# Optimization experiments

Hardware: AMD Instinct MI355X
Metric: run time of the kernel (lower is better)

## Reference

```python
import jax, jax.numpy as jnp
import numpy as np

N = 100000   # nodes
E = 600000   # edges
D = 128      # hidden_dim
R = 8        # edge_vocab_size (num_relations)
B = 64       # graphs in batch
V = 5000     # node_vocab_size
L = 3        # num_layers


def setup_inputs() -> dict:
    key = jax.random.key(0)
    ks = jax.random.split(key, 16)
    s = 1.0 / np.sqrt(D)
    node_type = jax.random.randint(ks[0], (N,), 0, V, dtype=jnp.int32)
    edge_index = jax.random.randint(ks[1], (2, E), 0, N, dtype=jnp.int32)
    edge_type = jax.random.randint(ks[2], (E,), 0, R, dtype=jnp.int32)
    batch = jnp.sort(jax.random.randint(ks[3], (N,), 0, B, dtype=jnp.int32))
    node_emb = jax.random.normal(ks[4], (V, D), dtype=jnp.float32)
    rel_w = jax.random.normal(ks[5], (L, R, D, D), dtype=jnp.float32) * s
    root_w = jax.random.normal(ks[6], (L, D, D), dtype=jnp.float32) * s
    bias = jnp.zeros((L, D), dtype=jnp.float32)
    risk_w1 = jax.random.normal(ks[7], (D, D), dtype=jnp.float32) * s
    risk_b1 = jnp.zeros((D,), dtype=jnp.float32)
    risk_w2 = jax.random.normal(ks[8], (D, 1), dtype=jnp.float32) * s
    risk_b2 = jnp.zeros((1,), dtype=jnp.float32)
    safe_w1 = jax.random.normal(ks[9], (D, D), dtype=jnp.float32) * s
    safe_b1 = jnp.zeros((D,), dtype=jnp.float32)
    safe_w2 = jax.random.normal(ks[10], (D, 1), dtype=jnp.float32) * s
    safe_b2 = jnp.zeros((1,), dtype=jnp.float32)
    return dict(node_type=node_type, edge_index=edge_index, edge_type=edge_type,
                batch=batch, node_emb=node_emb, rel_w=rel_w, root_w=root_w,
                bias=bias, risk_w1=risk_w1, risk_b1=risk_b1, risk_w2=risk_w2,
                risk_b2=risk_b2, safe_w1=safe_w1, safe_b1=safe_b1,
                safe_w2=safe_w2, safe_b2=safe_b2)


def _rgcn_layer(x, edge_index, edge_type, Wrel, Wroot, b):
    # PyG RGCNConv: per-relation mean aggregation of source features,
    # then relation-specific linear + root transform + bias.
    src, dst = edge_index[0], edge_index[1]
    seg = dst * R + edge_type                      # combined (node, relation) id
    msgs = x[src]                                  # [E, D] gather
    sums = jax.ops.segment_sum(msgs, seg, num_segments=N * R)      # [N*R, D]
    cnt = jax.ops.segment_sum(jnp.ones((E,), x.dtype), seg, num_segments=N * R)
    mean = sums / jnp.maximum(cnt, 1.0)[:, None]
    mean = mean.reshape(N, R, D)
    out = jnp.einsum('nrd,rde->ne', mean, Wrel) + x @ Wroot + b
    return out


def _mlp_head(g, w1, b1, w2, b2):
    h = jax.nn.relu(g @ w1 + b1)
    return (h @ w2 + b2).squeeze(-1)               # dropout is identity in eval


def reference(node_type, edge_index, edge_type, batch, node_emb, rel_w, root_w,
              bias, risk_w1, risk_b1, risk_w2, risk_b2, safe_w1, safe_b1,
              safe_w2, safe_b2):
    x = node_emb[node_type]                        # [N, D]
    for l in range(L):                             # fixed small layer loop
        x = jax.nn.relu(_rgcn_layer(x, edge_index, edge_type,
                                    rel_w[l], root_w[l], bias[l]))
    # global_mean_pool over graph ids
    g_sum = jax.ops.segment_sum(x, batch, num_segments=B)          # [B, D]
    g_cnt = jax.ops.segment_sum(jnp.ones((N,), x.dtype), batch, num_segments=B)
    g = g_sum / jnp.maximum(g_cnt, 1.0)[:, None]
    risk_pred = _mlp_head(g, risk_w1, risk_b1, risk_w2, risk_b2)   # [B]
    safe_logit = _mlp_head(g, safe_w1, safe_b1, safe_w2, safe_b2)  # [B]
    return risk_pred, safe_logit
```

## Files before the change

### kernel.cpp

```cpp
#include <hip/hip_runtime.h>
#include <hip/hip_bf16.h>

#define N_NODES 100000
#define N_EDGES 600000
#define DIM     128
#define N_REL   8
#define N_GRAPH 64
#define N_LAYER 3
#define NR      (N_NODES * N_REL)
#define OVF_CAP 16384

typedef __attribute__((ext_vector_type(4))) float float4v;
typedef __attribute__((ext_vector_type(2))) float float2v;
typedef unsigned long long ull;

__device__ __forceinline__ int gswz8(int row, int g) {
    return row * 16 + (g ^ (row & 15));
}

#define W8_TOTAL (N_LAYER * 9 * 8192)
#define PB_HIST  2344
#define PB_GATH  12500
#define PB_WPRE  864
#define PB_BCNT  1
#define PB_TOTAL (PB_HIST + PB_GATH + PB_WPRE + PB_BCNT)

__global__ __launch_bounds__(256) void k_prep(
    const int* __restrict__ ei, const int* __restrict__ et,
    int* __restrict__ cnt, int* __restrict__ srcs8,
    int* __restrict__ ovf, int* __restrict__ ovf_n,
    const int* __restrict__ nt, const float* __restrict__ emb, unsigned int* __restrict__ x8,
    const float* __restrict__ relw, const float* __restrict__ rootw,
    unsigned short* __restrict__ W8,
    const int* __restrict__ batch, int* __restrict__ gcnt)
{
    const int b = blockIdx.x, t = threadIdx.x;
    if (b < PB_HIST) {
        int e = b * 256 + t;
        if (e < N_EDGES) {
            int src = ei[e];
            int seg = ei[N_EDGES + e] * N_REL + et[e];
            int p = atomicAdd(&cnt[seg], 1);
            if (p < 8) {
                srcs8[seg * 8 + p] = src;
            } else {
                int q = atomicAdd(ovf_n, 1);
                if (q < OVF_CAP) { ovf[2 * q] = seg; ovf[2 * q + 1] = src; }
            }
        }
    } else if (b < PB_HIST + PB_GATH) {
        int gid = (b - PB_HIST) * 256 + t;
        int n = gid >> 5, up = gid & 31;
        const float* row = emb + (size_t)nt[n] * DIM;
        int p0 = up * 4;
        float f0 = row[((p0 + 0) & 7) * 16 + ((p0 + 0) >> 3)];
        float f1 = row[((p0 + 1) & 7) * 16 + ((p0 + 1) >> 3)];
        float f2 = row[((p0 + 2) & 7) * 16 + ((p0 + 2) >> 3)];
        float f3 = row[((p0 + 3) & 7) * 16 + ((p0 + 3) >> 3)];
        int u = __builtin_amdgcn_cvt_pk_fp8_f32(f0, f1, 0, false);
        u = __builtin_amdgcn_cvt_pk_fp8_f32(f2, f3, u, true);
        x8[gid] = (unsigned int)u;
    } else if (b < PB_HIST + PB_GATH + PB_WPRE) {
        int gid = (b - PB_HIST - PB_GATH) * 256 + t;
        int l = gid / (9 * 8192);
        int rem = gid - l * 9 * 8192;
        int r = rem >> 13;
        int idx = rem & 8191;
        int n = idx >> 6, p2 = idx & 63;
        int pos0 = 2 * p2, pos1 = 2 * p2 + 1;
        int k0 = (pos0 & 7) * 16 + (pos0 >> 3);
        int k1 = (pos1 & 7) * 16 + (pos1 >> 3);
        float w0, w1;
        if (r < 8) {
            const float* base = relw + ((size_t)(l * 8 + r) * 128) * 128 + n;
            w0 = base[(size_t)k0 * 128];
            w1 = base[(size_t)k1 * 128];
        } else {
            const float* base = rootw + (size_t)l * 128 * 128 + n;
            w0 = base[(size_t)k0 * 128];
            w1 = base[(size_t)k1 * 128];
        }
        int pk = __builtin_amdgcn_cvt_pk_fp8_f32(w0, w1, 0, false);
        W8[gid] = (unsigned short)(pk & 0xffff);
    } else {
        int g = t;
        if (g < N_GRAPH) {
            int lo = 0, hi = N_NODES;
            while (lo < hi) { int mid = (lo + hi) >> 1; if (batch[mid] < g) lo = mid + 1; else hi = mid; }
            int start = lo;
            lo = 0; hi = N_NODES;
            while (lo < hi) { int mid = (lo + hi) >> 1; if (batch[mid] < g + 1) lo = mid + 1; else hi = mid; }
            gcnt[g] = lo - start;
        }
    }
}

#define BM2 128
__global__ __launch_bounds__(256, 2) void k_gemm(
    const unsigned int* __restrict__ x8in,
    unsigned int* __restrict__ x8out,
    const unsigned short* __restrict__ W8,
    const float* __restrict__ bias,
    const int* __restrict__ cnt,
    const int* __restrict__ srcs8,
    const int* __restrict__ ovf,
    const int* __restrict__ ovf_n,
    const int* __restrict__ batch,
    float* __restrict__ gsum,
    int isLast)
{
    __shared__ __align__(16) ull Bls[4096];
    __shared__ __align__(16) ull Als[2048];
    const int t = threadIdx.x;
    const int wv = t >> 6, lane = t & 63;
    const int quad = lane >> 4, l15 = lane & 15;
    const int oct = lane >> 3, h = lane & 7;
    const int m0 = blockIdx.x * BM2;
    const int gn = m0 + wv * 32 + (lane >> 1);
    const int nodeC = (gn < N_NODES) ? gn : 0;
    const int f = lane & 1;

    float4v acc[2][8];
#pragma unroll
    for (int nt = 0; nt < 8; ++nt) {
        float bc = bias[nt * 16 + l15];
        acc[0][nt] = (float4v){bc, bc, bc, bc};
        acc[1][nt] = (float4v){bc, bc, bc, bc};
    }

    const ull* Xr = (const ull*)x8in;
    const uint4* x4p = (const uint4*)x8in;
    ull* AlsW = Als + wv * 512;
    uint4* Als4 = (uint4*)AlsW;

    ull bR[8], aR[8];
    uint4 u0[4], u1[4];
    int cc[4], s2v[4], s3v[4];

#define ACCUM(U) do {                                                  \
        A0 += __builtin_amdgcn_cvt_pk_f32_fp8((int)(U).x, false);      \
        A1 += __builtin_amdgcn_cvt_pk_f32_fp8((int)(U).x, true);       \
        A2 += __builtin_amdgcn_cvt_pk_f32_fp8((int)(U).y, false);      \
        A3 += __builtin_amdgcn_cvt_pk_f32_fp8((int)(U).y, true);       \
        A4 += __builtin_amdgcn_cvt_pk_f32_fp8((int)(U).z, false);      \
        A5 += __builtin_amdgcn_cvt_pk_f32_fp8((int)(U).z, true);       \
        A6 += __builtin_amdgcn_cvt_pk_f32_fp8((int)(U).w, false);      \
        A7 += __builtin_amdgcn_cvt_pk_f32_fp8((int)(U).w, true);       \
    } while (0)

    auto ld_meta = [&](int rr, int& cl, int& s0, int& s2) {
        int seg = nodeC * 8 + rr;
        cl = cnt[seg];
        s0 = srcs8[seg * 8 + f];
        s2 = srcs8[seg * 8 + 2 + f];
    };
    auto gat_issue = [&](int cl, int sl0, int sl2) {
#pragma unroll
        for (int nn = 0; nn < 4; ++nn) {
            int lw = nn * 8 + oct;
            cc[nn] = __shfl(cl, lw * 2);
            int s0 = __shfl(sl0, lw * 2);
            int s1 = __shfl(sl0, lw * 2 + 1);
            s2v[nn] = __shfl(sl2, lw * 2);
            s3v[nn] = __shfl(sl2, lw * 2 + 1);
            if (cc[nn] > 0) u0[nn] = x4p[(size_t)s0 * 8 + h];
            if (cc[nn] > 1) u1[nn] = x4p[(size_t)s1 * 8 + h];
        }
    };
    auto agg_consume = [&](int rr) {
        uint4 u2[4], u3[4];
#pragma unroll
        for (int nn = 0; nn < 4; ++nn) {
            if (cc[nn] > 2) u2[nn] = x4p[(size_t)s2v[nn] * 8 + h];
            if (cc[nn] > 3) u3[nn] = x4p[(size_t)s3v[nn] * 8 + h];
        }
#pragma unroll
        for (int nn = 0; nn < 4; ++nn) {
            int lw = nn * 8 + oct;
            float2v A0 = {0.f, 0.f}, A1 = {0.f, 0.f}, A2 = {0.f, 0.f}, A3 = {0.f, 0.f};
            float2v A4 = {0.f, 0.f}, A5 = {0.f, 0.f}, A6 = {0.f, 0.f}, A7 = {0.f, 0.f};
            if (cc[nn] > 0) ACCUM(u0[nn]);
            if (cc[nn] > 1) ACCUM(u1[nn]);
            if (cc[nn] > 2) ACCUM(u2[nn]);
            if (cc[nn] > 3) ACCUM(u3[nn]);
            if (cc[nn] > 4) {
                int seg = (m0 + wv * 32 + lw) * 8 + rr;
                int mc = cc[nn] < 8 ? cc[nn] : 8;
#pragma unroll 1
                for (int k = 4; k < mc; ++k) {
                    uint4 uu = x4p[(size_t)srcs8[seg * 8 + k] * 8 + h];
                    ACCUM(uu);
                }
                if (cc[nn] > 8) {
                    int ovn = ovf_n[0];
                    if (ovn > OVF_CAP) ovn = OVF_CAP;
#pragma unroll 1
                    for (int j = 0; j < ovn; ++j) {
                        if (ovf[2 * j] == seg) {
                            uint4 uu = x4p[(size_t)ovf[2 * j + 1] * 8 + h];
                            ACCUM(uu);
                        }
                    }
                }
            }
            float inv = (cc[nn] > 0) ? 1.0f / (float)cc[nn] : 0.f;
            float2v iv = {inv, inv};
            A0 *= iv; A1 *= iv; A2 *= iv; A3 *= iv;
            A4 *= iv; A5 *= iv; A6 *= iv; A7 *= iv;
            int w0 = __builtin_amdgcn_cvt_pk_fp8_f32(A0.x, A0.y, 0, false);
            w0 = __builtin_amdgcn_cvt_pk_fp8_f32(A1.x, A1.y, w0, true);
            int w1 = __builtin_amdgcn_cvt_pk_fp8_f32(A2.x, A2.y, 0, false);
            w1 = __builtin_amdgcn_cvt_pk_fp8_f32(A3.x, A3.y, w1, true);
            int w2 = __builtin_amdgcn_cvt_pk_fp8_f32(A4.x, A4.y, 0, false);
            w2 = __builtin_amdgcn_cvt_pk_fp8_f32(A5.x, A5.y, w2, true);
            int w3 = __builtin_amdgcn_cvt_pk_fp8_f32(A6.x, A6.y, 0, false);
            w3 = __builtin_amdgcn_cvt_pk_fp8_f32(A7.x, A7.y, w3, true);
            uint4 w; w.x = (unsigned int)w0; w.y = (unsigned int)w1;
            w.z = (unsigned int)w2; w.w = (unsigned int)w3;
            Als4[(lw >> 4) * 128 + h * 16 + ((lw & 15) ^ h)] = w;
        }
    };

    {
        const ull* Wc = (const ull*)W8;
#pragma unroll
        for (int i = 0; i < 8; ++i) bR[i] = Wc[t + 256 * i];
    }
    int clA, sl0A, sl2A, clN, sl0N, sl2N;
    ld_meta(0, clA, sl0A, sl2A);
    gat_issue(clA, sl0A, sl2A);
    ld_meta(1, clA, sl0A, sl2A);
#pragma unroll
    for (int i = 0; i < 8; ++i) {
        int idx = t + 256 * i;
        Bls[gswz8(idx >> 4, idx & 15)] = bR[i];
    }
    __syncthreads();

#pragma unroll
    for (int c = 0; c < 9; ++c) {
        const int cur = (c & 1) * 2048;
        if (c <= 7) agg_consume(c);
        if (c <= 5) ld_meta(c + 2, clN, sl0N, sl2N);
        if (c <= 6) gat_issue(clA, sl0A, sl2A);
        if (c < 8) {
            const ull* Wc = (const ull*)(W8 + (size_t)(c + 1) * 8192);
#pragma unroll
            for (int i = 0; i < 8; ++i) bR[i] = Wc[t + 256 * i];
        }
        if (c == 7) {
#pragma unroll
            for (int i = 0; i < 8; ++i) {
                int rt = i >> 2, kk = i & 3;
                aR[i] = Xr[(size_t)(m0 + wv * 32 + rt * 16 + l15) * 16 + kk * 4 + quad];
            }
        }
#pragma unroll
        for (int kk = 0; kk < 4; ++kk) {
            long long a0, a1;
            if (c == 8) {
                a0 = (long long)aR[kk];
                a1 = (long long)aR[4 + kk];
            } else {
                int j4 = kk * 4 + quad;
                int h2 = j4 >> 1, hf = j4 & 1;
                int slot = ((h2 * 16 + (l15 ^ h2)) << 1) | hf;
                a0 = (long long)AlsW[slot];
                a1 = (long long)AlsW[256 + slot];
            }
            int g = kk * 4 + quad;
#pragma unroll
            for (int nt = 0; nt < 8; ++nt) {
                long long b8 = (long long)Bls[cur + (nt * 16 + l15) * 16 + (g ^ l15)];
                acc[0][nt] = __builtin_amdgcn_mfma_f32_16x16x32_fp8_fp8(a0, b8, acc[0][nt], 0, 0, 0);
                acc[1][nt] = __builtin_amdgcn_mfma_f32_16x16x32_fp8_fp8(a1, b8, acc[1][nt], 0, 0, 0);
            }
        }
        if (c < 8) {
            const int nxt = ((c + 1) & 1) * 2048;
#pragma unroll
            for (int i = 0; i < 8; ++i) {
                int idx = t + 256 * i;
                Bls[nxt + gswz8(idx >> 4, idx & 15)] = bR[i];
            }
            __syncthreads();
        }
        clA = clN; sl0A = sl0N; sl2A = sl2N;
    }
#undef ACCUM

    if (!isLast) {
        ull* outs = (ull*)x8out;
#pragma unroll
        for (int rt = 0; rt < 2; ++rt) {
#pragma unroll
            for (int i = 0; i < 4; ++i) {
                int row = m0 + wv * 32 + rt * 16 + quad * 4 + i;
                float v0 = acc[rt][0][i], v1 = acc[rt][1][i];
                float v2 = acc[rt][2][i], v3 = acc[rt][3][i];
                float v4 = acc[rt][4][i], v5 = acc[rt][5][i];
                float v6 = acc[rt][6][i], v7 = acc[rt][7][i];
                v0 = v0 > 0.f ? v0 : 0.f;  v1 = v1 > 0.f ? v1 : 0.f;
                v2 = v2 > 0.f ? v2 : 0.f;  v3 = v3 > 0.f ? v3 : 0.f;
                v4 = v4 > 0.f ? v4 : 0.f;  v5 = v5 > 0.f ? v5 : 0.f;
                v6 = v6 > 0.f ? v6 : 0.f;  v7 = v7 > 0.f ? v7 : 0.f;
                int lo = __builtin_amdgcn_cvt_pk_fp8_f32(v0, v1, 0, false);
                lo = __builtin_amdgcn_cvt_pk_fp8_f32(v2, v3, lo, true);
                int hi = __builtin_amdgcn_cvt_pk_fp8_f32(v4, v5, 0, false);
                hi = __builtin_amdgcn_cvt_pk_fp8_f32(v6, v7, hi, true);
                if (row < N_NODES) {
                    ull w = ((ull)(unsigned int)hi << 32) | (unsigned int)lo;
                    outs[(size_t)row * 16 + l15] = w;
                }
            }
        }
    } else {
        float s[8];
#pragma unroll
        for (int nt = 0; nt < 8; ++nt) s[nt] = 0.f;
        int curg = -1;
#pragma unroll
        for (int rt = 0; rt < 2; ++rt) {
#pragma unroll
            for (int i = 0; i < 4; ++i) {
                int row = m0 + wv * 32 + rt * 16 + quad * 4 + i;
                if (row < N_NODES) {
                    int gb = batch[row];
                    if (gb != curg) {
                        if (curg >= 0) {
#pragma unroll
                            for (int nt = 0; nt < 8; ++nt)
                                atomicAdd(&gsum[curg * 128 + nt * 16 + l15], s[nt]);
#pragma unroll
                            for (int nt = 0; nt < 8; ++nt) s[nt] = 0.f;
                        }
                        curg = gb;
                    }
#pragma unroll
                    for (int nt = 0; nt < 8; ++nt) {
                        float v = acc[rt][nt][i];
                        s[nt] += v > 0.f ? v : 0.f;
                    }
                }
            }
        }
        if (curg >= 0) {
#pragma unroll
            for (int nt = 0; nt < 8; ++nt)
                atomicAdd(&gsum[curg * 128 + nt * 16 + l15], s[nt]);
        }
    }
}

__global__ __launch_bounds__(128) void k_heads(
    const float* __restrict__ gsum, const int* __restrict__ gcnt,
    const float* __restrict__ rw1, const float* __restrict__ rb1,
    const float* __restrict__ rw2, const float* __restrict__ rb2,
    const float* __restrict__ sw1, const float* __restrict__ sb1,
    const float* __restrict__ sw2, const float* __restrict__ sb2,
    float* __restrict__ out) {
    __shared__ float g[128];
    __shared__ float parts[2];
    int b = blockIdx.x, t = threadIdx.x;
    int c = gcnt[b];
    float invc = 1.0f / (float)(c > 0 ? c : 1);
    g[t] = gsum[b * 128 + t] * invc;
    __syncthreads();
    float acc = rb1[t];
    for (int d = 0; d < 128; ++d) acc += g[d] * rw1[d * 128 + t];
    float h = acc > 0.f ? acc : 0.f;
    float p = h * rw2[t];
    for (int o = 32; o > 0; o >>= 1) p += __shfl_down(p, o);
    if ((t & 63) == 0) parts[t >> 6] = p;
    __syncthreads();
    if (t == 0) out[b] = parts[0] + parts[1] + rb2[0];
    __syncthreads();
    acc = sb1[t];
    for (int d = 0; d < 128; ++d) acc += g[d] * sw1[d * 128 + t];
    h = acc > 0.f ? acc : 0.f;
    p = h * sw2[t];
    for (int o = 32; o > 0; o >>= 1) p += __shfl_down(p, o);
    if ((t & 63) == 0) parts[t >> 6] = p;
    __syncthreads();
    if (t == 0) out[64 + b] = parts[0] + parts[1] + sb2[0];
}

extern "C" void kernel_launch(void* const* d_in, const int* in_sizes, int n_in,
                              void* d_out, int out_size, void* d_ws, size_t ws_size,
                              hipStream_t stream) {
    const int*   node_type  = (const int*)d_in[0];
    const int*   edge_index = (const int*)d_in[1];
    const int*   edge_type  = (const int*)d_in[2];
    const int*   batch      = (const int*)d_in[3];
    const float* node_emb   = (const float*)d_in[4];
    const float* rel_w      = (const float*)d_in[5];
    const float* root_w     = (const float*)d_in[6];
    const float* bias       = (const float*)d_in[7];
    const float* rw1        = (const float*)d_in[8];
    const float* rb1        = (const float*)d_in[9];
    const float* rw2        = (const float*)d_in[10];
    const float* rb2        = (const float*)d_in[11];
    const float* sw1        = (const float*)d_in[12];
    const float* sb1        = (const float*)d_in[13];
    const float* sw2        = (const float*)d_in[14];
    const float* sb2        = (const float*)d_in[15];
    float* out = (float*)d_out;

    char* ws = (char*)d_ws;
    size_t off = 0;
    auto alloc = [&](size_t bytes) -> void* {
        void* p = ws + off;
        off += (bytes + 255) & ~(size_t)255;
        return p;
    };
    unsigned int*   x8a    = (unsigned int*)alloc((size_t)N_NODES * 32 * 4);
    unsigned int*   x8b    = (unsigned int*)alloc((size_t)N_NODES * 32 * 4);
    int*            cnt    = (int*)alloc((size_t)NR * 4);
    int*            srcs8  = (int*)alloc((size_t)NR * 8 * 4);
    int*            ovf    = (int*)alloc((size_t)OVF_CAP * 2 * 4);
    unsigned short* W8     = (unsigned short*)alloc((size_t)W8_TOTAL * 2);
    float*          gsum   = (float*)alloc((64 * 128 + 64 + 64) * 4);
    int*            gcnt   = (int*)(gsum + 64 * 128);
    int*            ovf_n  = (int*)(gsum + 64 * 128 + 64);
    if (off > ws_size) return;

    hipMemsetAsync(cnt, 0, (size_t)NR * 4, stream);
    hipMemsetAsync(gsum, 0, (size_t)(64 * 128 + 64 + 64) * 4, stream);
    k_prep<<<PB_TOTAL, 256, 0, stream>>>(edge_index, edge_type, cnt, srcs8, ovf, ovf_n,
                                         node_type, node_emb, x8a,
                                         rel_w, root_w, W8, batch, gcnt);

    unsigned int* xcur = x8a;
    unsigned int* xnext = x8b;
    const int gb = (N_NODES + BM2 - 1) / BM2;
    for (int l = 0; l < N_LAYER; ++l) {
        const unsigned short* W8l = W8 + (size_t)l * 9 * 8192;
        const float* bl = bias + (size_t)l * 128;
        k_gemm<<<gb, 256, 0, stream>>>(xcur, xnext, W8l, bl, cnt, srcs8, ovf, ovf_n,
                                       batch, gsum, (l == N_LAYER - 1) ? 1 : 0);
        unsigned int* tmp = xcur; xcur = xnext; xnext = tmp;
    }

    k_heads<<<64, 128, 0, stream>>>(gsum, gcnt, rw1, rb1, rw2, rb2,
                                    sw1, sb1, sw2, sb2, out);
}
```

Before: 401.3 us.

## Split prep kernel and pre-reduce graph pooling sums in shared memory

The combined prep kernel is split into two launches: one for the edge histogram and bucketing, one for the embedding gather and weight preformat. The last layer's mean-pool epilogue now accumulates per-graph partial sums in LDS when a tile spans fewer than four graphs. It then issues one global atomic per nonzero element, which should cut global atomic traffic on gsum. The cost is an extra kernel launch plus added barriers and LDS atomics in the epilogue.

```diff
diff --git a/kernel.cpp b/kernel.cpp
--- a/kernel.cpp
+++ b/kernel.cpp
@@ -23,33 +23,35 @@
 #define PB_GATH  12500
 #define PB_WPRE  864
 #define PB_BCNT  1
-#define PB_TOTAL (PB_HIST + PB_GATH + PB_WPRE + PB_BCNT)
-
-__global__ __launch_bounds__(256) void k_prep(
+
+__global__ __launch_bounds__(256) void k_prep_edges(
     const int* __restrict__ ei, const int* __restrict__ et,
     int* __restrict__ cnt, int* __restrict__ srcs8,
-    int* __restrict__ ovf, int* __restrict__ ovf_n,
+    int* __restrict__ ovf, int* __restrict__ ovf_n)
+{
+    int e = blockIdx.x * 256 + threadIdx.x;
+    if (e < N_EDGES) {
+        int src = ei[e];
+        int seg = ei[N_EDGES + e] * N_REL + et[e];
+        int p = atomicAdd(&cnt[seg], 1);
+        if (p < 8) {
+            srcs8[seg * 8 + p] = src;
+        } else {
+            int q = atomicAdd(ovf_n, 1);
+            if (q < OVF_CAP) { ovf[2 * q] = seg; ovf[2 * q + 1] = src; }
+        }
+    }
+}
+
+__global__ __launch_bounds__(256) void k_prep_rest(
     const int* __restrict__ nt, const float* __restrict__ emb, unsigned int* __restrict__ x8,
     const float* __restrict__ relw, const float* __restrict__ rootw,
     unsigned short* __restrict__ W8,
     const int* __restrict__ batch, int* __restrict__ gcnt)
 {
     const int b = blockIdx.x, t = threadIdx.x;
-    if (b < PB_HIST) {
-        int e = b * 256 + t;
-        if (e < N_EDGES) {
-            int src = ei[e];
-            int seg = ei[N_EDGES + e] * N_REL + et[e];
-            int p = atomicAdd(&cnt[seg], 1);
-            if (p < 8) {
-                srcs8[seg * 8 + p] = src;
-            } else {
-                int q = atomicAdd(ovf_n, 1);
-                if (q < OVF_CAP) { ovf[2 * q] = seg; ovf[2 * q + 1] = src; }
-            }
-        }
-    } else if (b < PB_HIST + PB_GATH) {
-        int gid = (b - PB_HIST) * 256 + t;
+    if (b < PB_GATH) {
+        int gid = b * 256 + t;
         int n = gid >> 5, up = gid & 31;
         const float* row = emb + (size_t)nt[n] * DIM;
         int p0 = up * 4;
@@ -60,8 +62,8 @@
         int u = __builtin_amdgcn_cvt_pk_fp8_f32(f0, f1, 0, false);
         u = __builtin_amdgcn_cvt_pk_fp8_f32(f2, f3, u, true);
         x8[gid] = (unsigned int)u;
-    } else if (b < PB_HIST + PB_GATH + PB_WPRE) {
-        int gid = (b - PB_HIST - PB_GATH) * 256 + t;
+    } else if (b < PB_GATH + PB_WPRE) {
+        int gid = (b - PB_GATH) * 256 + t;
         int l = gid / (9 * 8192);
         int rem = gid - l * 9 * 8192;
         int r = rem >> 13;
@@ -315,6 +317,13 @@
             }
         }
     } else {
+        __syncthreads();
+        float* gred = (float*)Bls;
+        for (int k2 = t; k2 < 512; k2 += 256) gred[k2] = 0.f;
+        __syncthreads();
+        int r1 = m0 + BM2 - 1; if (r1 >= N_NODES) r1 = N_NODES - 1;
+        const int gLo = batch[m0];
+        const bool fits = (batch[r1] - gLo) < 4;
         float s[8];
 #pragma unroll
         for (int nt = 0; nt < 8; ++nt) s[nt] = 0.f;
@@ -328,9 +337,15 @@
                     int gb = batch[row];
                     if (gb != curg) {
                         if (curg >= 0) {
-#pragma unroll
-                            for (int nt = 0; nt < 8; ++nt)
-                                atomicAdd(&gsum[curg * 128 + nt * 16 + l15], s[nt]);
+                            if (fits) {
+#pragma unroll
+                                for (int nt = 0; nt < 8; ++nt)
+                                    if (s[nt] != 0.f) atomicAdd(&gred[(curg - gLo) * 128 + nt * 16 + l15], s[nt]);
+                            } else {
+#pragma unroll
+                                for (int nt = 0; nt < 8; ++nt)
+                                    atomicAdd(&gsum[curg * 128 + nt * 16 + l15], s[nt]);
+                            }
 #pragma unroll
                             for (int nt = 0; nt < 8; ++nt) s[nt] = 0.f;
                         }
@@ -345,9 +360,23 @@
             }
         }
         if (curg >= 0) {
-#pragma unroll
-            for (int nt = 0; nt < 8; ++nt)
-                atomicAdd(&gsum[curg * 128 + nt * 16 + l15], s[nt]);
+            if (fits) {
+#pragma unroll
+                for (int nt = 0; nt < 8; ++nt)
+                    if (s[nt] != 0.f) atomicAdd(&gred[(curg - gLo) * 128 + nt * 16 + l15], s[nt]);
+            } else {
+#pragma unroll
+                for (int nt = 0; nt < 8; ++nt)
+                    atomicAdd(&gsum[curg * 128 + nt * 16 + l15], s[nt]);
+            }
+        }
+        __syncthreads();
+        if (fits) {
+            for (int k2 = t; k2 < 512; k2 += 256) {
+                float v = gred[k2];
+                if (v != 0.f)
+                    atomicAdd(&gsum[(gLo + (k2 >> 7)) * 128 + (k2 & 127)], v);
+            }
         }
     }
 }
@@ -426,9 +455,9 @@
 
     hipMemsetAsync(cnt, 0, (size_t)NR * 4, stream);
     hipMemsetAsync(gsum, 0, (size_t)(64 * 128 + 64 + 64) * 4, stream);
-    k_prep<<<PB_TOTAL, 256, 0, stream>>>(edge_index, edge_type, cnt, srcs8, ovf, ovf_n,
-                                         node_type, node_emb, x8a,
-                                         rel_w, root_w, W8, batch, gcnt);
+    k_prep_edges<<<PB_HIST, 256, 0, stream>>>(edge_index, edge_type, cnt, srcs8, ovf, ovf_n);
+    k_prep_rest<<<PB_GATH + PB_WPRE + PB_BCNT, 256, 0, stream>>>(node_type, node_emb, x8a,
+                                                                 rel_w, root_w, W8, batch, gcnt);
 
     unsigned int* xcur = x8a;
     unsigned int* xnext = x8b;
```

Measured after the change: 365.7 us (median of 2 runs). -8.9%, faster.

## Load FP8 weight fragments straight into registers, drop LDS staging, pool in LDS

Applied to the files above, without the earlier changes.

The weights are pre-swizzled into MFMA B-operand fragment order in the prep kernel. Each wave then loads its B fragments directly from global/L2 into double-buffered registers, which removes the B staging buffer in shared memory and the per-chunk __syncthreads. The last-layer graph pooling first accumulates into a small shared-memory buffer when a block spans few graphs, which cuts global atomics. The two memsets are also merged into one. In exchange, every wave now reloads the weights redundantly from cache, and register pressure goes up.

```diff
diff --git a/kernel.cpp b/kernel.cpp
--- a/kernel.cpp
+++ b/kernel.cpp
@@ -13,10 +13,6 @@
 typedef __attribute__((ext_vector_type(4))) float float4v;
 typedef __attribute__((ext_vector_type(2))) float float2v;
 typedef unsigned long long ull;
-
-__device__ __forceinline__ int gswz8(int row, int g) {
-    return row * 16 + (g ^ (row & 15));
-}
 
 #define W8_TOTAL (N_LAYER * 9 * 8192)
 #define PB_HIST  2344
@@ -64,15 +60,23 @@
         int gid = (b - PB_HIST - PB_GATH) * 256 + t;
         int l = gid / (9 * 8192);
         int rem = gid - l * 9 * 8192;
-        int r = rem >> 13;
+        int c = rem >> 13;
         int idx = rem & 8191;
-        int n = idx >> 6, p2 = idx & 63;
+        int pp = idx & 3;
+        int fu = idx >> 2;
+        int lane = fu & 63;
+        int kkNt = fu >> 6;
+        int kk = kkNt >> 3, ntc = kkNt & 7;
+        int quad = lane >> 4, l15 = lane & 15;
+        int n = ntc * 16 + l15;
+        int g = kk * 4 + quad;
+        int p2 = g * 4 + pp;
         int pos0 = 2 * p2, pos1 = 2 * p2 + 1;
         int k0 = (pos0 & 7) * 16 + (pos0 >> 3);
         int k1 = (pos1 & 7) * 16 + (pos1 >> 3);
         float w0, w1;
-        if (r < 8) {
-            const float* base = relw + ((size_t)(l * 8 + r) * 128) * 128 + n;
+        if (c < 8) {
+            const float* base = relw + ((size_t)(l * 8 + c) * 128) * 128 + n;
             w0 = base[(size_t)k0 * 128];
             w1 = base[(size_t)k1 * 128];
         } else {
@@ -96,6 +100,7 @@
 }
 
 #define BM2 128
+#define WCH 2048
 __global__ __launch_bounds__(256, 2) void k_gemm(
     const unsigned int* __restrict__ x8in,
     unsigned int* __restrict__ x8out,
@@ -109,7 +114,6 @@
     float* __restrict__ gsum,
     int isLast)
 {
-    __shared__ __align__(16) ull Bls[4096];
     __shared__ __align__(16) ull Als[2048];
     const int t = threadIdx.x;
     const int wv = t >> 6, lane = t & 63;
@@ -120,6 +124,14 @@
     const int nodeC = (gn < N_NODES) ? gn : 0;
     const int f = lane & 1;
 
+    const ull* Wf = (const ull*)W8;
+
+    ull bWa[8], bWb[8];
+#pragma unroll
+    for (int i = 0; i < 8; ++i) bWa[i] = Wf[(i << 6) + lane];
+#pragma unroll
+    for (int i = 0; i < 8; ++i) bWb[i] = Wf[512 + (i << 6) + lane];
+
     float4v acc[2][8];
 #pragma unroll
     for (int nt = 0; nt < 8; ++nt) {
@@ -133,7 +145,7 @@
     ull* AlsW = Als + wv * 512;
     uint4* Als4 = (uint4*)AlsW;
 
-    ull bR[8], aR[8];
+    ull aR[8];
     uint4 u0[4], u1[4];
     int cc[4], s2v[4], s3v[4];
 
@@ -221,33 +233,16 @@
         }
     };
 
-    {
-        const ull* Wc = (const ull*)W8;
-#pragma unroll
-        for (int i = 0; i < 8; ++i) bR[i] = Wc[t + 256 * i];
-    }
     int clA, sl0A, sl2A, clN, sl0N, sl2N;
     ld_meta(0, clA, sl0A, sl2A);
     gat_issue(clA, sl0A, sl2A);
     ld_meta(1, clA, sl0A, sl2A);
-#pragma unroll
-    for (int i = 0; i < 8; ++i) {
-        int idx = t + 256 * i;
-        Bls[gswz8(idx >> 4, idx & 15)] = bR[i];
-    }
-    __syncthreads();
 
 #pragma unroll
     for (int c = 0; c < 9; ++c) {
-        const int cur = (c & 1) * 2048;
         if (c <= 7) agg_consume(c);
         if (c <= 5) ld_meta(c + 2, clN, sl0N, sl2N);
         if (c <= 6) gat_issue(clA, sl0A, sl2A);
-        if (c < 8) {
-            const ull* Wc = (const ull*)(W8 + (size_t)(c + 1) * 8192);
-#pragma unroll
-            for (int i = 0; i < 8; ++i) bR[i] = Wc[t + 256 * i];
-        }
         if (c == 7) {
 #pragma unroll
             for (int i = 0; i < 8; ++i) {
@@ -257,6 +252,7 @@
         }
 #pragma unroll
         for (int kk = 0; kk < 4; ++kk) {
+            const int s = c * 4 + kk;
             long long a0, a1;
             if (c == 8) {
                 a0 = (long long)aR[kk];
@@ -268,22 +264,30 @@
                 a0 = (long long)AlsW[slot];
                 a1 = (long long)AlsW[256 + slot];
             }
-            int g = kk * 4 + quad;
-#pragma unroll
-            for (int nt = 0; nt < 8; ++nt) {
-                long long b8 = (long long)Bls[cur + (nt * 16 + l15) * 16 + (g ^ l15)];
-                acc[0][nt] = __builtin_amdgcn_mfma_f32_16x16x32_fp8_fp8(a0, b8, acc[0][nt], 0, 0, 0);
-                acc[1][nt] = __builtin_amdgcn_mfma_f32_16x16x32_fp8_fp8(a1, b8, acc[1][nt], 0, 0, 0);
-            }
-        }
-        if (c < 8) {
-            const int nxt = ((c + 1) & 1) * 2048;
-#pragma unroll
-            for (int i = 0; i < 8; ++i) {
-                int idx = t + 256 * i;
-                Bls[nxt + gswz8(idx >> 4, idx & 15)] = bR[i];
-            }
-            __syncthreads();
+            if ((s & 1) == 0) {
+#pragma unroll
+                for (int nt = 0; nt < 8; ++nt) {
+                    acc[0][nt] = __builtin_amdgcn_mfma_f32_16x16x32_fp8_fp8(a0, (long long)bWa[nt], acc[0][nt], 0, 0, 0);
+                    acc[1][nt] = __builtin_amdgcn_mfma_f32_16x16x32_fp8_fp8(a1, (long long)bWa[nt], acc[1][nt], 0, 0, 0);
+                }
+            } else {
+#pragma unroll
+                for (int nt = 0; nt < 8; ++nt) {
+                    acc[0][nt] = __builtin_amdgcn_mfma_f32_16x16x32_fp8_fp8(a0, (long long)bWb[nt], acc[0][nt], 0, 0, 0);
+                    acc[1][nt] = __builtin_amdgcn_mfma_f32_16x16x32_fp8_fp8(a1, (long long)bWb[nt], acc[1][nt], 0, 0, 0);
+                }
+            }
+            if (s + 2 < 36) {
+                const int s2 = s + 2;
+                const ull* Wc = Wf + (size_t)(s2 >> 2) * WCH + ((s2 & 3) << 9);
+                if ((s & 1) == 0) {
+#pragma unroll
+                    for (int i = 0; i < 8; ++i) bWa[i] = Wc[(i << 6) + lane];
+                } else {
+#pragma unroll
+                    for (int i = 0; i < 8; ++i) bWb[i] = Wc[(i << 6) + lane];
+                }
+            }
         }
         clA = clN; sl0A = sl0N; sl2A = sl2N;
     }
@@ -315,6 +319,13 @@
             }
         }
     } else {
+        __syncthreads();
+        float* gred = (float*)Als;
+        for (int k2 = t; k2 < 512; k2 += 256) gred[k2] = 0.f;
+        __syncthreads();
+        int r1 = m0 + BM2 - 1; if (r1 >= N_NODES) r1 = N_NODES - 1;
+        const int gLo = batch[m0];
+        const bool fits = (batch[r1] - gLo) < 4;
         float s[8];
 #pragma unroll
         for (int nt = 0; nt < 8; ++nt) s[nt] = 0.f;
@@ -328,9 +339,15 @@
                     int gb = batch[row];
                     if (gb != curg) {
                         if (curg >= 0) {
-#pragma unroll
-                            for (int nt = 0; nt < 8; ++nt)
-                                atomicAdd(&gsum[curg * 128 + nt * 16 + l15], s[nt]);
+                            if (fits) {
+#pragma unroll
+                                for (int nt = 0; nt < 8; ++nt)
+                                    if (s[nt] != 0.f) atomicAdd(&gred[(curg - gLo) * 128 + nt * 16 + l15], s[nt]);
+                            } else {
+#pragma unroll
+                                for (int nt = 0; nt < 8; ++nt)
+                                    atomicAdd(&gsum[curg * 128 + nt * 16 + l15], s[nt]);
+                            }
 #pragma unroll
                             for (int nt = 0; nt < 8; ++nt) s[nt] = 0.f;
                         }
@@ -345,9 +362,23 @@
             }
         }
         if (curg >= 0) {
-#pragma unroll
-            for (int nt = 0; nt < 8; ++nt)
-                atomicAdd(&gsum[curg * 128 + nt * 16 + l15], s[nt]);
+            if (fits) {
+#pragma unroll
+                for (int nt = 0; nt < 8; ++nt)
+                    if (s[nt] != 0.f) atomicAdd(&gred[(curg - gLo) * 128 + nt * 16 + l15], s[nt]);
+            } else {
+#pragma unroll
+                for (int nt = 0; nt < 8; ++nt)
+                    atomicAdd(&gsum[curg * 128 + nt * 16 + l15], s[nt]);
+            }
+        }
+        __syncthreads();
+        if (fits) {
+            for (int k2 = t; k2 < 512; k2 += 256) {
+                float v = gred[k2];
+                if (v != 0.f)
+                    atomicAdd(&gsum[(gLo + (k2 >> 7)) * 128 + (k2 & 127)], v);
+            }
         }
     }
 }
@@ -415,17 +446,17 @@
     };
     unsigned int*   x8a    = (unsigned int*)alloc((size_t)N_NODES * 32 * 4);
     unsigned int*   x8b    = (unsigned int*)alloc((size_t)N_NODES * 32 * 4);
-    int*            cnt    = (int*)alloc((size_t)NR * 4);
+    const size_t ZWORDS = (size_t)NR + 64 * 128 + 64 + 64;
+    int*            cnt    = (int*)alloc(ZWORDS * 4);
+    float*          gsum   = (float*)(cnt + NR);
+    int*            gcnt   = (int*)(gsum + 64 * 128);
+    int*            ovf_n  = gcnt + 64;
     int*            srcs8  = (int*)alloc((size_t)NR * 8 * 4);
     int*            ovf    = (int*)alloc((size_t)OVF_CAP * 2 * 4);
     unsigned short* W8     = (unsigned short*)alloc((size_t)W8_TOTAL * 2);
-    float*          gsum   = (float*)alloc((64 * 128 + 64 + 64) * 4);
-    int*            gcnt   = (int*)(gsum + 64 * 128);
-    int*            ovf_n  = (int*)(gsum + 64 * 128 + 64);
     if (off > ws_size) return;
 
-    hipMemsetAsync(cnt, 0, (size_t)NR * 4, stream);
-    hipMemsetAsync(gsum, 0, (size_t)(64 * 128 + 64 + 64) * 4, stream);
+    hipMemsetAsync(cnt, 0, ZWORDS * 4, stream);
     k_prep<<<PB_TOTAL, 256, 0, stream>>>(edge_index, edge_type, cnt, srcs8, ovf, ovf_n,
                                          node_type, node_emb, x8a,
                                          rel_w, root_w, W8, batch, gcnt);
```

After: 380.3 us. 5.2% less time.
